# Kernel optimization log

Measured on AMD Instinct MI355X. Metric: run time of the kernel, lower is better.

Reference implementation:

```python
import jax, jax.numpy as jnp
import numpy as np

EMBED_DIM = 1024
NUM_HEADS = 16
HEAD_DIM = EMBED_DIM // NUM_HEADS  # 64, used only for score scaling
B, S = 4, 2048


def setup_inputs() -> dict:
    key = jax.random.key(0)
    k1, k2, k3, k4 = jax.random.split(key, 4)
    rotation_params = jax.random.normal(k1, (3 * EMBED_DIM * EMBED_DIM,), dtype=jnp.float32) * 0.02
    entangle_params = jax.random.normal(k2, (EMBED_DIM * EMBED_DIM,), dtype=jnp.float32) * 0.02
    inputs = jax.random.normal(k3, (B, S, EMBED_DIM), dtype=jnp.float32)
    gate_w = jax.random.normal(k4, (EMBED_DIM, EMBED_DIM), dtype=jnp.float32) * 0.02
    return {"rotation_params": rotation_params, "entangle_params": entangle_params,
            "inputs": inputs, "gate_w": gate_w}


def reference(rotation_params, entangle_params, inputs, gate_w):
    E = EMBED_DIM
    w_qkv = rotation_params.reshape(3 * E, E)   # nn.Linear weight layout (out, in)
    w_out = entangle_params.reshape(E, E)
    # qkv projection: x @ W^T, then chunk into q, k, v along last dim
    qkv = jnp.einsum('bse,fe->bsf', inputs, w_qkv)  # (B, S, 3E)
    q, k, v = jnp.split(qkv, 3, axis=-1)
    # NOTE: original code does NOT split into heads; attention over full E,
    # scaled by sqrt(head_dim).
    q = q * (1.0 / np.sqrt(HEAD_DIM)).astype(np.float32)
    scores = jnp.einsum('bqe,bke->bqk', q, k)       # (B, S, S)
    attn = jax.nn.softmax(scores, axis=-1)
    attn_out = jnp.einsum('bqk,bke->bqe', attn, v)  # (B, S, E)
    out = jnp.einsum('bse,fe->bsf', attn_out, w_out)
    gate = jax.nn.sigmoid(jnp.einsum('bse,fe->bsf', out, gate_w))
    return gate * out
```

## Files before the change

### kernel.cpp

```cpp
#include <hip/hip_runtime.h>
#include <math.h>

#define EMB 1024
#define NB 4
#define SQ 2048
#define TOK (NB*SQ)

typedef __attribute__((ext_vector_type(8))) short bhalf8;
typedef __attribute__((ext_vector_type(4))) float f32x4;

__device__ __forceinline__ unsigned short f32_to_bf16(float f) {
    unsigned int u = __float_as_uint(f);
    u += 0x7FFFu + ((u >> 16) & 1u);
    return (unsigned short)(u >> 16);
}
__device__ __forceinline__ float bf16_to_f32(unsigned short h) {
    return __uint_as_float(((unsigned int)h) << 16);
}

__global__ __launch_bounds__(256) void convert_kernel(const float* __restrict__ src,
                                                      unsigned short* __restrict__ dst,
                                                      int n4, float scale) {
    int i = blockIdx.x * 256 + threadIdx.x;
    if (i >= n4) return;
    float4 v = ((const float4*)src)[i];
    ushort4 o;
    o.x = f32_to_bf16(v.x * scale);
    o.y = f32_to_bf16(v.y * scale);
    o.z = f32_to_bf16(v.z * scale);
    o.w = f32_to_bf16(v.w * scale);
    ((ushort4*)dst)[i] = o;
}

__global__ __launch_bounds__(256) void convert_weights_kernel(
    const float* __restrict__ rot, const float* __restrict__ ent,
    const float* __restrict__ gw, unsigned short* __restrict__ dst) {
    const int i = blockIdx.x * 256 + threadIdx.x;
    const int EE4 = EMB * EMB / 4;
    const float* src;
    float scale = 1.0f;
    int j = i;
    if (i < 3 * EE4) {
        src = rot;
        if (i < EE4) scale = 0.125f;
    } else if (i < 4 * EE4) { src = ent; j = i - 3 * EE4; }
    else                    { src = gw;  j = i - 4 * EE4; }
    float4 v = ((const float4*)src)[j];
    ushort4 o;
    o.x = f32_to_bf16(v.x * scale);
    o.y = f32_to_bf16(v.y * scale);
    o.z = f32_to_bf16(v.z * scale);
    o.w = f32_to_bf16(v.w * scale);
    ((ushort4*)dst)[i] = o;
}

__device__ __forceinline__ void async_load16(const unsigned short* gp, unsigned short* lp) {
    __builtin_amdgcn_global_load_lds(
        (const __attribute__((address_space(1))) unsigned int*)gp,
        (__attribute__((address_space(3))) unsigned int*)lp,
        16, 0, 0);
}

template <int MODE>
__global__ __launch_bounds__(256) void gemm_nt(
    const unsigned short* __restrict__ A,
    const unsigned short* __restrict__ B,
    void* __restrict__ C,
    const float* __restrict__ Ofp,
    float* __restrict__ Fout,
    int M, int N, int K, int lda, int ldb, int ldc,
    long sA, long sB, long sC)
{
    __shared__ __align__(16) unsigned short As[128*64];
    __shared__ __align__(16) unsigned short Bs[128*64];

    const int bz = blockIdx.z;
    const unsigned short* Ab = A + (long)bz * sA;
    const unsigned short* Bb = B + (long)bz * sB;
    const int bm = blockIdx.x * 128;
    const int bn = blockIdx.y * 128;
    const int t = threadIdx.x;
    const int w = t >> 6;
    const int l = t & 63;
    const int srow8 = l >> 3;
    const int scol  = (((l & 7) ^ ((l >> 3) & 7)) * 8);

    f32x4 zero = {0.f, 0.f, 0.f, 0.f};
    f32x4 acc[4][4];
    #pragma unroll
    for (int i = 0; i < 4; ++i)
        #pragma unroll
        for (int j = 0; j < 4; ++j) acc[i][j] = zero;

    const int wm = (w >> 1) * 64;
    const int wn = (w & 1) * 64;
    const int fr = l & 15;
    const int kqs0 = ((((l >> 4)    ) ^ (l & 7)) * 8);
    const int kqs1 = (((4 + (l >> 4)) ^ (l & 7)) * 8);

    const int nkt = K >> 6;
    for (int kt = 0; kt < nkt; ++kt) {
        const int k0 = kt << 6;
        __syncthreads();
        #pragma unroll
        for (int r = 0; r < 4; ++r) {
            const int rr = (r*4 + w) * 8 + srow8;
            async_load16(Ab + (long)(bm + rr) * lda + (k0 + scol), As + (r*4 + w) * 512);
            async_load16(Bb + (long)(bn + rr) * ldb + (k0 + scol), Bs + (r*4 + w) * 512);
        }
        __syncthreads();

        #pragma unroll
        for (int h = 0; h < 2; ++h) {
            const int kq = h ? kqs1 : kqs0;
            bhalf8 af[4], bfr[4];
            #pragma unroll
            for (int mi = 0; mi < 4; ++mi)
                af[mi] = *(const bhalf8*)(As + (wm + mi*16 + fr) * 64 + kq);
            #pragma unroll
            for (int ni = 0; ni < 4; ++ni)
                bfr[ni] = *(const bhalf8*)(Bs + (wn + ni*16 + fr) * 64 + kq);
            #pragma unroll
            for (int mi = 0; mi < 4; ++mi)
                #pragma unroll
                for (int ni = 0; ni < 4; ++ni)
                    acc[mi][ni] = __builtin_amdgcn_mfma_f32_16x16x32_bf16(
                        af[mi], bfr[ni], acc[mi][ni], 0, 0, 0);
        }
    }

    const int crow = (l >> 4) * 4;
    const int ccol = l & 15;
    #pragma unroll
    for (int mi = 0; mi < 4; ++mi) {
        #pragma unroll
        for (int ni = 0; ni < 4; ++ni) {
            #pragma unroll
            for (int r = 0; r < 4; ++r) {
                const int gr = bm + wm + mi*16 + crow + r;
                const int gc = bn + wn + ni*16 + ccol;
                const float v = acc[mi][ni][r];
                const long idx = (long)gr * ldc + gc;
                if (MODE == 0) {
                    ((unsigned short*)C)[(long)bz*sC + idx] = f32_to_bf16(v);
                } else if (MODE == 1) {
                    ((float*)C)[(long)bz*sC + idx] = v;
                } else if (MODE == 2) {
                    const float o = Ofp[idx];
                    const float g = 1.0f / (1.0f + __expf(-v));
                    Fout[idx] = g * o;
                } else {
                    ((unsigned short*)C)[idx] = f32_to_bf16(v);
                    Fout[idx] = v;
                }
            }
        }
    }
}

__global__ __launch_bounds__(256) void softmax_kernel(const float* __restrict__ sc,
                                                      unsigned short* __restrict__ attn) {
    const long row = blockIdx.x;
    const float* p = sc + row * SQ;
    unsigned short* q = attn + row * SQ;
    const int t = threadIdx.x;
    const int w = t >> 6, l = t & 63;
    float4 a = ((const float4*)p)[2*t];
    float4 b = ((const float4*)p)[2*t + 1];
    float f[8] = {a.x, a.y, a.z, a.w, b.x, b.y, b.z, b.w};
    float m = -1e30f;
    #pragma unroll
    for (int j = 0; j < 8; ++j) m = fmaxf(m, f[j]);
    #pragma unroll
    for (int off = 32; off; off >>= 1) m = fmaxf(m, __shfl_xor(m, off));
    __shared__ float smax[4], ssum[4];
    if (l == 0) smax[w] = m;
    __syncthreads();
    m = fmaxf(fmaxf(smax[0], smax[1]), fmaxf(smax[2], smax[3]));
    float s = 0.f;
    #pragma unroll
    for (int j = 0; j < 8; ++j) { f[j] = __expf(f[j] - m); s += f[j]; }
    #pragma unroll
    for (int off = 32; off; off >>= 1) s += __shfl_xor(s, off);
    if (l == 0) ssum[w] = s;
    __syncthreads();
    const float inv = 1.0f / (ssum[0] + ssum[1] + ssum[2] + ssum[3]);
    union { bhalf8 v; unsigned short u[8]; } o;
    #pragma unroll
    for (int j = 0; j < 8; ++j) o.u[j] = f32_to_bf16(f[j] * inv);
    ((bhalf8*)q)[t] = o.v;
}

__global__ void transpose_v(const unsigned short* __restrict__ qkv,
                            unsigned short* __restrict__ vT) {
    __shared__ unsigned short tile[32][33];
    const int b = blockIdx.z;
    const unsigned short* v = qkv + (long)b * SQ * (3*EMB) + 2*EMB;
    const int e = blockIdx.x * 32 + threadIdx.x;
    const int s = blockIdx.y * 32 + threadIdx.y;
    tile[threadIdx.y][threadIdx.x] = v[(long)s * (3*EMB) + e];
    __syncthreads();
    const int so = blockIdx.y * 32 + threadIdx.x;
    const int eo = blockIdx.x * 32 + threadIdx.y;
    vT[(long)b * EMB * SQ + (long)eo * SQ + so] = tile[threadIdx.x][threadIdx.y];
}

extern "C" void kernel_launch(void* const* d_in, const int* in_sizes, int n_in,
                              void* d_out, int out_size, void* d_ws, size_t ws_size,
                              hipStream_t stream) {
    const float* rot = (const float*)d_in[0];
    const float* ent = (const float*)d_in[1];
    const float* x   = (const float*)d_in[2];
    const float* gw  = (const float*)d_in[3];
    float* outp = (float*)d_out;
    char* ws = (char*)d_ws;

    size_t off = 0;
    unsigned short* x_bf    = (unsigned short*)(ws + off); off += (size_t)TOK*EMB*2;
    unsigned short* wqkv_bf = (unsigned short*)(ws + off); off += (size_t)3*EMB*EMB*2;
    unsigned short* wout_bf = (unsigned short*)(ws + off); off += (size_t)EMB*EMB*2;
    unsigned short* gate_bf = (unsigned short*)(ws + off); off += (size_t)EMB*EMB*2;
    unsigned short* qkv_bf  = (unsigned short*)(ws + off); off += (size_t)TOK*3*EMB*2;
    unsigned short* vT_bf   = (unsigned short*)(ws + off); off += (size_t)NB*EMB*SQ*2;
    float*          sc_f32  = (float*)(ws + off);          off += (size_t)NB*SQ*SQ*4;
    unsigned short* attn_bf = qkv_bf;
    unsigned short* ao_bf   = x_bf;
    unsigned short* out_bf  = qkv_bf + (size_t)NB*SQ*SQ;
    float*          out_f32 = sc_f32;

    convert_kernel<<<dim3(TOK*EMB/4/256), dim3(256), 0, stream>>>(x, x_bf, TOK*EMB/4, 1.0f);
    convert_weights_kernel<<<dim3(5*EMB*EMB/4/256), dim3(256), 0, stream>>>(rot, ent, gw, wqkv_bf);

    gemm_nt<0><<<dim3(TOK/128, 3*EMB/128, 1), dim3(256), 0, stream>>>(
        x_bf, wqkv_bf, qkv_bf, nullptr, nullptr,
        TOK, 3*EMB, EMB, EMB, EMB, 3*EMB, 0, 0, 0);

    transpose_v<<<dim3(EMB/32, SQ/32, NB), dim3(32, 32), 0, stream>>>(qkv_bf, vT_bf);

    gemm_nt<1><<<dim3(SQ/128, SQ/128, NB), dim3(256), 0, stream>>>(
        qkv_bf, qkv_bf + EMB, sc_f32, nullptr, nullptr,
        SQ, SQ, EMB, 3*EMB, 3*EMB, SQ,
        (long)SQ*3*EMB, (long)SQ*3*EMB, (long)SQ*SQ);

    softmax_kernel<<<dim3(NB*SQ), dim3(256), 0, stream>>>(sc_f32, attn_bf);

    gemm_nt<0><<<dim3(SQ/128, EMB/128, NB), dim3(256), 0, stream>>>(
        attn_bf, vT_bf, ao_bf, nullptr, nullptr,
        SQ, EMB, SQ, SQ, SQ, EMB,
        (long)SQ*SQ, (long)EMB*SQ, (long)SQ*EMB);

    gemm_nt<3><<<dim3(TOK/128, EMB/128, 1), dim3(256), 0, stream>>>(
        ao_bf, wout_bf, out_bf, nullptr, out_f32,
        TOK, EMB, EMB, EMB, EMB, EMB, 0, 0, 0);

    gemm_nt<2><<<dim3(TOK/128, EMB/128, 1), dim3(256), 0, stream>>>(
        out_bf, gate_bf, nullptr, out_f32, outp,
        TOK, EMB, EMB, EMB, EMB, EMB, 0, 0, 0);
}
```

Measured before the change: 346.8 us.

## Use 32x32 MFMA tiles, store scores in fp16, merge conversion kernels

The GEMM kernel switches from 16x16x32 to 32x32x16 bf16 MFMA instructions, with a 2x2 grid of 32x32 accumulators per wave. This cuts LDS fragment loads per MFMA and raises math density. Attention scores are now written as fp16 instead of fp32, halving the traffic into and out of the softmax, at the cost of some score precision. The two fp32-to-bf16 conversion kernels become a single launch.

```diff
diff --git a/kernel.cpp b/kernel.cpp
--- a/kernel.cpp
+++ b/kernel.cpp
@@ -8,6 +8,7 @@
 
 typedef __attribute__((ext_vector_type(8))) short bhalf8;
 typedef __attribute__((ext_vector_type(4))) float f32x4;
+typedef __attribute__((ext_vector_type(16))) float f32x16;
 
 __device__ __forceinline__ unsigned short f32_to_bf16(float f) {
     unsigned int u = __float_as_uint(f);
@@ -17,29 +18,31 @@
 __device__ __forceinline__ float bf16_to_f32(unsigned short h) {
     return __uint_as_float(((unsigned int)h) << 16);
 }
-
-__global__ __launch_bounds__(256) void convert_kernel(const float* __restrict__ src,
-                                                      unsigned short* __restrict__ dst,
-                                                      int n4, float scale) {
-    int i = blockIdx.x * 256 + threadIdx.x;
-    if (i >= n4) return;
-    float4 v = ((const float4*)src)[i];
-    ushort4 o;
-    o.x = f32_to_bf16(v.x * scale);
-    o.y = f32_to_bf16(v.y * scale);
-    o.z = f32_to_bf16(v.z * scale);
-    o.w = f32_to_bf16(v.w * scale);
-    ((ushort4*)dst)[i] = o;
-}
-
-__global__ __launch_bounds__(256) void convert_weights_kernel(
+__device__ __forceinline__ unsigned short f32_to_f16(float f) {
+    union { _Float16 h; unsigned short u; } c; c.h = (_Float16)f; return c.u;
+}
+__device__ __forceinline__ float f16_to_f32(unsigned short u) {
+    union { _Float16 h; unsigned short u; } c; c.u = u; return (float)c.h;
+}
+
+__global__ __launch_bounds__(256) void convert_all_kernel(
+    const float* __restrict__ x,  unsigned short* __restrict__ x_bf,
     const float* __restrict__ rot, const float* __restrict__ ent,
-    const float* __restrict__ gw, unsigned short* __restrict__ dst) {
-    const int i = blockIdx.x * 256 + threadIdx.x;
+    const float* __restrict__ gw, unsigned short* __restrict__ w_bf) {
     const int EE4 = EMB * EMB / 4;
     const float* src;
+    unsigned short* dst;
     float scale = 1.0f;
-    int j = i;
+    int j;
+    if (blockIdx.x < TOK*EMB/4/256) {
+        src = x; dst = x_bf; j = blockIdx.x * 256 + threadIdx.x;
+        float4 v = ((const float4*)src)[j];
+        ushort4 o = { f32_to_bf16(v.x), f32_to_bf16(v.y), f32_to_bf16(v.z), f32_to_bf16(v.w) };
+        ((ushort4*)dst)[j] = o;
+        return;
+    }
+    const int i = (blockIdx.x - TOK*EMB/4/256) * 256 + threadIdx.x;
+    j = i; dst = w_bf;
     if (i < 3 * EE4) {
         src = rot;
         if (i < EE4) scale = 0.125f;
@@ -85,18 +88,22 @@
     const int srow8 = l >> 3;
     const int scol  = (((l & 7) ^ ((l >> 3) & 7)) * 8);
 
-    f32x4 zero = {0.f, 0.f, 0.f, 0.f};
-    f32x4 acc[4][4];
-    #pragma unroll
-    for (int i = 0; i < 4; ++i)
-        #pragma unroll
-        for (int j = 0; j < 4; ++j) acc[i][j] = zero;
+    f32x16 acc[2][2];
+    #pragma unroll
+    for (int i = 0; i < 2; ++i)
+        #pragma unroll
+        for (int j = 0; j < 2; ++j)
+            #pragma unroll
+            for (int r = 0; r < 16; ++r) acc[i][j][r] = 0.f;
 
     const int wm = (w >> 1) * 64;
     const int wn = (w & 1) * 64;
-    const int fr = l & 15;
-    const int kqs0 = ((((l >> 4)    ) ^ (l & 7)) * 8);
-    const int kqs1 = (((4 + (l >> 4)) ^ (l & 7)) * 8);
+    const int m31 = l & 31;
+    const int half = l >> 5;
+    int kq[4];
+    #pragma unroll
+    for (int ks = 0; ks < 4; ++ks)
+        kq[ks] = (((ks*2 + half) ^ (l & 7)) * 8);
 
     const int nkt = K >> 6;
     for (int kt = 0; kt < nkt; ++kt) {
@@ -111,40 +118,40 @@
         __syncthreads();
 
         #pragma unroll
-        for (int h = 0; h < 2; ++h) {
-            const int kq = h ? kqs1 : kqs0;
-            bhalf8 af[4], bfr[4];
-            #pragma unroll
-            for (int mi = 0; mi < 4; ++mi)
-                af[mi] = *(const bhalf8*)(As + (wm + mi*16 + fr) * 64 + kq);
-            #pragma unroll
-            for (int ni = 0; ni < 4; ++ni)
-                bfr[ni] = *(const bhalf8*)(Bs + (wn + ni*16 + fr) * 64 + kq);
-            #pragma unroll
-            for (int mi = 0; mi < 4; ++mi)
+        for (int ks = 0; ks < 4; ++ks) {
+            bhalf8 af[2], bfr[2];
+            #pragma unroll
+            for (int mi = 0; mi < 2; ++mi)
+                af[mi] = *(const bhalf8*)(As + (wm + mi*32 + m31) * 64 + kq[ks]);
+            #pragma unroll
+            for (int ni = 0; ni < 2; ++ni)
+                bfr[ni] = *(const bhalf8*)(Bs + (wn + ni*32 + m31) * 64 + kq[ks]);
+            #pragma unroll
+            for (int mi = 0; mi < 2; ++mi)
                 #pragma unroll
-                for (int ni = 0; ni < 4; ++ni)
-                    acc[mi][ni] = __builtin_amdgcn_mfma_f32_16x16x32_bf16(
+                for (int ni = 0; ni < 2; ++ni)
+                    acc[mi][ni] = __builtin_amdgcn_mfma_f32_32x32x16_bf16(
                         af[mi], bfr[ni], acc[mi][ni], 0, 0, 0);
         }
     }
 
-    const int crow = (l >> 4) * 4;
-    const int ccol = l & 15;
-    #pragma unroll
-    for (int mi = 0; mi < 4; ++mi) {
-        #pragma unroll
-        for (int ni = 0; ni < 4; ++ni) {
-            #pragma unroll
-            for (int r = 0; r < 4; ++r) {
-                const int gr = bm + wm + mi*16 + crow + r;
-                const int gc = bn + wn + ni*16 + ccol;
+    const int ccol = m31;
+    const int rbase = half * 4;
+    #pragma unroll
+    for (int mi = 0; mi < 2; ++mi) {
+        #pragma unroll
+        for (int ni = 0; ni < 2; ++ni) {
+            #pragma unroll
+            for (int r = 0; r < 16; ++r) {
+                const int row = (r & 3) + 8 * (r >> 2) + rbase;
+                const int gr = bm + wm + mi*32 + row;
+                const int gc = bn + wn + ni*32 + ccol;
                 const float v = acc[mi][ni][r];
                 const long idx = (long)gr * ldc + gc;
                 if (MODE == 0) {
                     ((unsigned short*)C)[(long)bz*sC + idx] = f32_to_bf16(v);
                 } else if (MODE == 1) {
-                    ((float*)C)[(long)bz*sC + idx] = v;
+                    ((unsigned short*)C)[(long)bz*sC + idx] = f32_to_f16(v);
                 } else if (MODE == 2) {
                     const float o = Ofp[idx];
                     const float g = 1.0f / (1.0f + __expf(-v));
@@ -158,19 +165,19 @@
     }
 }
 
-__global__ __launch_bounds__(256) void softmax_kernel(const float* __restrict__ sc,
+__global__ __launch_bounds__(256) void softmax_kernel(const unsigned short* __restrict__ sc,
                                                       unsigned short* __restrict__ attn) {
     const long row = blockIdx.x;
-    const float* p = sc + row * SQ;
+    const unsigned short* p = sc + row * SQ;
     unsigned short* q = attn + row * SQ;
     const int t = threadIdx.x;
     const int w = t >> 6, l = t & 63;
-    float4 a = ((const float4*)p)[2*t];
-    float4 b = ((const float4*)p)[2*t + 1];
-    float f[8] = {a.x, a.y, a.z, a.w, b.x, b.y, b.z, b.w};
+    union { bhalf8 v; unsigned short u[8]; } in;
+    in.v = ((const bhalf8*)p)[t];
+    float f[8];
     float m = -1e30f;
     #pragma unroll
-    for (int j = 0; j < 8; ++j) m = fmaxf(m, f[j]);
+    for (int j = 0; j < 8; ++j) { f[j] = f16_to_f32(in.u[j]); m = fmaxf(m, f[j]); }
     #pragma unroll
     for (int off = 32; off; off >>= 1) m = fmaxf(m, __shfl_xor(m, off));
     __shared__ float smax[4], ssum[4];
@@ -222,14 +229,15 @@
     unsigned short* gate_bf = (unsigned short*)(ws + off); off += (size_t)EMB*EMB*2;
     unsigned short* qkv_bf  = (unsigned short*)(ws + off); off += (size_t)TOK*3*EMB*2;
     unsigned short* vT_bf   = (unsigned short*)(ws + off); off += (size_t)NB*EMB*SQ*2;
-    float*          sc_f32  = (float*)(ws + off);          off += (size_t)NB*SQ*SQ*4;
+    char*           scbase  = (char*)(ws + off);           off += (size_t)NB*SQ*SQ*4;
+    unsigned short* sc_f16  = (unsigned short*)scbase;
+    float*          out_f32 = (float*)scbase;
     unsigned short* attn_bf = qkv_bf;
     unsigned short* ao_bf   = x_bf;
     unsigned short* out_bf  = qkv_bf + (size_t)NB*SQ*SQ;
-    float*          out_f32 = sc_f32;
-
-    convert_kernel<<<dim3(TOK*EMB/4/256), dim3(256), 0, stream>>>(x, x_bf, TOK*EMB/4, 1.0f);
-    convert_weights_kernel<<<dim3(5*EMB*EMB/4/256), dim3(256), 0, stream>>>(rot, ent, gw, wqkv_bf);
+
+    convert_all_kernel<<<dim3(TOK*EMB/4/256 + 5*EMB*EMB/4/256), dim3(256), 0, stream>>>(
+        x, x_bf, rot, ent, gw, wqkv_bf);
 
     gemm_nt<0><<<dim3(TOK/128, 3*EMB/128, 1), dim3(256), 0, stream>>>(
         x_bf, wqkv_bf, qkv_bf, nullptr, nullptr,
@@ -238,11 +246,11 @@
     transpose_v<<<dim3(EMB/32, SQ/32, NB), dim3(32, 32), 0, stream>>>(qkv_bf, vT_bf);
 
     gemm_nt<1><<<dim3(SQ/128, SQ/128, NB), dim3(256), 0, stream>>>(
-        qkv_bf, qkv_bf + EMB, sc_f32, nullptr, nullptr,
+        qkv_bf, qkv_bf + EMB, sc_f16, nullptr, nullptr,
         SQ, SQ, EMB, 3*EMB, 3*EMB, SQ,
         (long)SQ*3*EMB, (long)SQ*3*EMB, (long)SQ*SQ);
 
-    softmax_kernel<<<dim3(NB*SQ), dim3(256), 0, stream>>>(sc_f32, attn_bf);
+    softmax_kernel<<<dim3(NB*SQ), dim3(256), 0, stream>>>(sc_f16, attn_bf);
 
     gemm_nt<0><<<dim3(SQ/128, EMB/128, NB), dim3(256), 0, stream>>>(
         attn_bf, vT_bf, ao_bf, nullptr, nullptr,
```

After: 324.7 us. 6.4% less time.
